# Performance work log

Hardware: AMD Instinct MI355X
Metric: run time of the kernel (lower is better)

The kernel has to match this reference:

```python
import jax, jax.numpy as jnp
import numpy as np

N1 = 100000  # layer-1 target nodes
N2 = 10000   # layer-2 target (batch) nodes
HIDDEN = 16  # hardcoded in SAGENet.__init__


def _sage_layer(x_src, src, dst, n_tgt, W, b):
    # gather neighbor messages, mean-aggregate per target, then linear
    msgs = x_src[src]                                   # [E, d]
    summed = jax.ops.segment_sum(msgs, dst, num_segments=n_tgt)  # [n_tgt, d]
    cnt = jax.ops.segment_sum(jnp.ones((src.shape[0], 1), x_src.dtype), dst,
                              num_segments=n_tgt)       # [n_tgt, 1]
    mean = summed / jnp.maximum(cnt, 1.0)
    return mean @ W + b


def setup_inputs() -> dict:
    key = jax.random.key(0)
    ks = jax.random.split(key, 9)
    in_ch, out_ch = 128, 64
    N0, E1, E2 = 500000, 2000000, 400000
    x = jax.random.normal(ks[0], (N0, in_ch), dtype=jnp.float32)
    src1 = jax.random.randint(ks[1], (E1,), 0, N0)
    dst1 = jax.random.randint(ks[2], (E1,), 0, N1)
    src2 = jax.random.randint(ks[3], (E2,), 0, N1)
    dst2 = jax.random.randint(ks[4], (E2,), 0, N2)
    # Glorot-ish init for the two SAGE linear layers
    W1 = jax.random.normal(ks[5], (in_ch, HIDDEN), dtype=jnp.float32) / np.sqrt(in_ch)
    b1 = jnp.zeros((HIDDEN,), dtype=jnp.float32)
    W2 = jax.random.normal(ks[6], (HIDDEN, out_ch), dtype=jnp.float32) / np.sqrt(HIDDEN)
    b2 = jnp.zeros((out_ch,), dtype=jnp.float32)
    return {"x": x, "W1": W1, "b1": b1, "W2": W2, "b2": b2,
            "src1": src1, "dst1": dst1, "src2": src2, "dst2": dst2}


def reference(x, W1, b1, W2, b2, src1, dst1, src2, dst2):
    # layer 1: bipartite SAGE conv (no root term since x_r is None) + relu
    h1 = jax.nn.relu(_sage_layer(x, src1, dst1, N1, W1, b1))      # [N1, 16]
    # dropout is a no-op in eval mode
    # layer 2
    h2 = _sage_layer(h1, src2, dst2, N2, W2, b2)                  # [N2, 64]
    return jax.nn.log_softmax(h2, axis=1)
```

## Files before the change

### kernel.cpp

```cpp
#include <hip/hip_runtime.h>
#include <hip/hip_bf16.h>

#define IN_CH 128
#define HID   16
#define N1_T  100000
#define N2_T  10000
#define OUT_CH 64

constexpr int PROJ_ROWS = 64;
constexpr int XS_STRIDE = 132;

__global__ __launch_bounds__(256) void proj_kernel(
    const float* __restrict__ x, const float* __restrict__ W1,
    float* __restrict__ xp, int n0) {
  __shared__ float xs[PROJ_ROWS * XS_STRIDE];

  const int tid = threadIdx.x;
  const int rowBase = blockIdx.x * PROJ_ROWS;

  const float4* x4 = reinterpret_cast<const float4*>(x + (size_t)rowBase * IN_CH);
  #pragma unroll
  for (int i = 0; i < 8; ++i) {
    int f = tid + i * 256;
    int r = f >> 5;
    int c4 = f & 31;
    if (rowBase + r < n0) {
      *reinterpret_cast<float4*>(&xs[r * XS_STRIDE + c4 * 4]) = x4[f];
    }
  }
  __syncthreads();

  const int lane = tid & 63;
  const int c0 = __builtin_amdgcn_readfirstlane((tid >> 6) << 2);

  const float* xrow = &xs[lane * XS_STRIDE];
  float a0 = 0.f, a1 = 0.f, a2 = 0.f, a3 = 0.f;
  #pragma unroll
  for (int k = 0; k < IN_CH; k += 4) {
    float4 xv = *reinterpret_cast<const float4*>(xrow + k);
    float4 w0 = *reinterpret_cast<const float4*>(W1 + (k + 0) * HID + c0);
    float4 w1 = *reinterpret_cast<const float4*>(W1 + (k + 1) * HID + c0);
    float4 w2 = *reinterpret_cast<const float4*>(W1 + (k + 2) * HID + c0);
    float4 w3 = *reinterpret_cast<const float4*>(W1 + (k + 3) * HID + c0);
    a0 += xv.x * w0.x + xv.y * w1.x + xv.z * w2.x + xv.w * w3.x;
    a1 += xv.x * w0.y + xv.y * w1.y + xv.z * w2.y + xv.w * w3.y;
    a2 += xv.x * w0.z + xv.y * w1.z + xv.z * w2.z + xv.w * w3.z;
    a3 += xv.x * w0.w + xv.y * w1.w + xv.z * w2.w + xv.w * w3.w;
  }

  const int orow = rowBase + lane;
  if (orow < n0) {
    *reinterpret_cast<float4*>(&xp[(size_t)orow * HID + c0]) =
        make_float4(a0, a1, a2, a3);
  }
}

__global__ __launch_bounds__(256) void build_list(
    const int* __restrict__ dst, int E, int* head, int* __restrict__ nxt) {
  const int stride = gridDim.x * blockDim.x;
  for (int t = blockIdx.x * blockDim.x + threadIdx.x; t < E; t += stride) {
    const int d = dst[t];
    const int old = atomicExch(&head[d], t);
    nxt[t] = old;
  }
}

__global__ __launch_bounds__(256) void agg_layer(
    const float* __restrict__ feat, const int* __restrict__ srcArr,
    const int* __restrict__ head, const int* __restrict__ nxt,
    const float* __restrict__ bias, float* __restrict__ outFeat,
    int nrows, int doReluBias) {
  const int gid = blockIdx.x * blockDim.x + threadIdx.x;
  const int row = gid >> 2;
  const int q = gid & 3;
  if (row >= nrows) return;

  int e = head[row];
  float4 acc = make_float4(0.f, 0.f, 0.f, 0.f);
  int cnt = 0;
  while (e >= 0) {
    const int s = srcArr[e];
    const float4 v =
        *reinterpret_cast<const float4*>(&feat[(size_t)s * HID + q * 4]);
    acc.x += v.x; acc.y += v.y; acc.z += v.z; acc.w += v.w;
    ++cnt;
    e = nxt[e];
  }
  const float inv = 1.0f / (float)(cnt > 0 ? cnt : 1);
  float4 r;
  r.x = acc.x * inv; r.y = acc.y * inv; r.z = acc.z * inv; r.w = acc.w * inv;
  if (doReluBias) {
    const float4 b = reinterpret_cast<const float4*>(bias)[q];
    r.x = fmaxf(r.x + b.x, 0.f);
    r.y = fmaxf(r.y + b.y, 0.f);
    r.z = fmaxf(r.z + b.z, 0.f);
    r.w = fmaxf(r.w + b.w, 0.f);
  }
  *reinterpret_cast<float4*>(&outFeat[(size_t)row * HID + q * 4]) = r;
}

__global__ __launch_bounds__(256) void out_kernel(
    const float* __restrict__ mean2, const float* __restrict__ W2,
    const float* __restrict__ b2, float* __restrict__ out, int n2) {
  const int row = blockIdx.x * 4 + (threadIdx.x >> 6);
  if (row >= n2) return;
  const int c = threadIdx.x & 63;

  float acc = b2[c];
  #pragma unroll
  for (int k = 0; k < HID; ++k) {
    acc += mean2[(size_t)row * HID + k] * W2[k * OUT_CH + c];
  }
  float mx = acc;
  #pragma unroll
  for (int off = 32; off > 0; off >>= 1) mx = fmaxf(mx, __shfl_xor(mx, off));
  float ex = expf(acc - mx);
  float sum = ex;
  #pragma unroll
  for (int off = 32; off > 0; off >>= 1) sum += __shfl_xor(sum, off);
  out[(size_t)row * OUT_CH + c] = acc - mx - logf(sum);
}

extern "C" void kernel_launch(void* const* d_in, const int* in_sizes, int n_in,
                              void* d_out, int out_size, void* d_ws, size_t ws_size,
                              hipStream_t stream) {
  const float* x   = (const float*)d_in[0];
  const float* W1  = (const float*)d_in[1];
  const float* b1  = (const float*)d_in[2];
  const float* W2  = (const float*)d_in[3];
  const float* b2  = (const float*)d_in[4];
  const int* src1  = (const int*)d_in[5];
  const int* dst1  = (const int*)d_in[6];
  const int* src2  = (const int*)d_in[7];
  const int* dst2  = (const int*)d_in[8];

  const int n0 = in_sizes[0] / IN_CH;
  const int E1 = in_sizes[5];
  const int E2 = in_sizes[7];

  float* ws    = (float*)d_ws;
  float* xp    = ws;
  float* h1    = xp + (size_t)n0 * HID;
  float* mean2 = h1 + (size_t)N1_T * HID;
  int*   head  = (int*)(mean2 + (size_t)N2_T * HID);
  int*   nxt1  = head + (N1_T + N2_T);
  int*   nxt2  = nxt1 + E1;

  float* out = (float*)d_out;

  hipMemsetAsync(head, 0xFF, (size_t)(N1_T + N2_T) * sizeof(int), stream);

  build_list<<<1024, 256, 0, stream>>>(dst1, E1, head, nxt1);
  build_list<<<256, 256, 0, stream>>>(dst2, E2, head + N1_T, nxt2);

  const int proj_blocks = (n0 + PROJ_ROWS - 1) / PROJ_ROWS;
  proj_kernel<<<proj_blocks, 256, 0, stream>>>(x, W1, xp, n0);

  agg_layer<<<(N1_T * 4 + 255) / 256, 256, 0, stream>>>(
      xp, src1, head, nxt1, b1, h1, N1_T, 1);

  agg_layer<<<(N2_T * 4 + 255) / 256, 256, 0, stream>>>(
      h1, src2, head + N1_T, nxt2, nullptr, mean2, N2_T, 0);

  out_kernel<<<(N2_T + 3) / 4, 256, 0, stream>>>(mean2, W2, b2, out, N2_T);
}
```

Baseline: 609.0 us.

## Restructure projection: stage transposed W1 in LDS, read x directly per thread

The projection kernel no longer stages x tiles in shared memory. It loads a transposed copy of W1 into LDS, and each thread reads four x rows straight from global memory to compute a 4x4 output tile. Each block now covers 256 rows instead of 64. The aim is to drop the x staging and barrier cost and to reuse weights from LDS across four rows. The risk is that lanes read x rows 512 bytes apart, so global loads may coalesce worse than the contiguous float4 tile load did.

```diff
diff --git a/kernel.cpp b/kernel.cpp
--- a/kernel.cpp
+++ b/kernel.cpp
@@ -7,52 +7,81 @@
 #define N2_T  10000
 #define OUT_CH 64
 
-constexpr int PROJ_ROWS = 64;
-constexpr int XS_STRIDE = 132;
+constexpr int WT_STRIDE = 132;
 
 __global__ __launch_bounds__(256) void proj_kernel(
     const float* __restrict__ x, const float* __restrict__ W1,
     float* __restrict__ xp, int n0) {
-  __shared__ float xs[PROJ_ROWS * XS_STRIDE];
+  __shared__ float wt[HID * WT_STRIDE];
 
   const int tid = threadIdx.x;
-  const int rowBase = blockIdx.x * PROJ_ROWS;
 
-  const float4* x4 = reinterpret_cast<const float4*>(x + (size_t)rowBase * IN_CH);
-  #pragma unroll
-  for (int i = 0; i < 8; ++i) {
-    int f = tid + i * 256;
-    int r = f >> 5;
-    int c4 = f & 31;
-    if (rowBase + r < n0) {
-      *reinterpret_cast<float4*>(&xs[r * XS_STRIDE + c4 * 4]) = x4[f];
-    }
+  if (tid < IN_CH) {
+    const float4* wrow = reinterpret_cast<const float4*>(W1 + tid * HID);
+    float4 w0 = wrow[0], w1 = wrow[1], w2 = wrow[2], w3 = wrow[3];
+    wt[ 0 * WT_STRIDE + tid] = w0.x; wt[ 1 * WT_STRIDE + tid] = w0.y;
+    wt[ 2 * WT_STRIDE + tid] = w0.z; wt[ 3 * WT_STRIDE + tid] = w0.w;
+    wt[ 4 * WT_STRIDE + tid] = w1.x; wt[ 5 * WT_STRIDE + tid] = w1.y;
+    wt[ 6 * WT_STRIDE + tid] = w1.z; wt[ 7 * WT_STRIDE + tid] = w1.w;
+    wt[ 8 * WT_STRIDE + tid] = w2.x; wt[ 9 * WT_STRIDE + tid] = w2.y;
+    wt[10 * WT_STRIDE + tid] = w2.z; wt[11 * WT_STRIDE + tid] = w2.w;
+    wt[12 * WT_STRIDE + tid] = w3.x; wt[13 * WT_STRIDE + tid] = w3.y;
+    wt[14 * WT_STRIDE + tid] = w3.z; wt[15 * WT_STRIDE + tid] = w3.w;
   }
   __syncthreads();
 
-  const int lane = tid & 63;
-  const int c0 = __builtin_amdgcn_readfirstlane((tid >> 6) << 2);
+  const int q = tid & 3;
+  const int g = tid >> 2;
+  const int r0 = blockIdx.x * 256 + g * 4;
+  if (r0 >= n0) return;
 
-  const float* xrow = &xs[lane * XS_STRIDE];
-  float a0 = 0.f, a1 = 0.f, a2 = 0.f, a3 = 0.f;
-  #pragma unroll
-  for (int k = 0; k < IN_CH; k += 4) {
-    float4 xv = *reinterpret_cast<const float4*>(xrow + k);
-    float4 w0 = *reinterpret_cast<const float4*>(W1 + (k + 0) * HID + c0);
-    float4 w1 = *reinterpret_cast<const float4*>(W1 + (k + 1) * HID + c0);
-    float4 w2 = *reinterpret_cast<const float4*>(W1 + (k + 2) * HID + c0);
-    float4 w3 = *reinterpret_cast<const float4*>(W1 + (k + 3) * HID + c0);
-    a0 += xv.x * w0.x + xv.y * w1.x + xv.z * w2.x + xv.w * w3.x;
-    a1 += xv.x * w0.y + xv.y * w1.y + xv.z * w2.y + xv.w * w3.y;
-    a2 += xv.x * w0.z + xv.y * w1.z + xv.z * w2.z + xv.w * w3.z;
-    a3 += xv.x * w0.w + xv.y * w1.w + xv.z * w2.w + xv.w * w3.w;
+  const float* wq = &wt[(q * 4) * WT_STRIDE];
+  const float* xr0 = x + (size_t)r0 * IN_CH;
+  const float* xr1 = x + (size_t)min(r0 + 1, n0 - 1) * IN_CH;
+  const float* xr2 = x + (size_t)min(r0 + 2, n0 - 1) * IN_CH;
+  const float* xr3 = x + (size_t)min(r0 + 3, n0 - 1) * IN_CH;
+
+  float4 acc0 = make_float4(0.f, 0.f, 0.f, 0.f);
+  float4 acc1 = acc0, acc2 = acc0, acc3 = acc0;
+
+  #pragma unroll 8
+  for (int kb = 0; kb < IN_CH; kb += 4) {
+    const float4 wa = *reinterpret_cast<const float4*>(wq + 0 * WT_STRIDE + kb);
+    const float4 wb = *reinterpret_cast<const float4*>(wq + 1 * WT_STRIDE + kb);
+    const float4 wc = *reinterpret_cast<const float4*>(wq + 2 * WT_STRIDE + kb);
+    const float4 wd = *reinterpret_cast<const float4*>(wq + 3 * WT_STRIDE + kb);
+    const float4 x0 = *reinterpret_cast<const float4*>(xr0 + kb);
+    const float4 x1 = *reinterpret_cast<const float4*>(xr1 + kb);
+    const float4 x2 = *reinterpret_cast<const float4*>(xr2 + kb);
+    const float4 x3 = *reinterpret_cast<const float4*>(xr3 + kb);
+
+    acc0.x += x0.x*wa.x + x0.y*wa.y + x0.z*wa.z + x0.w*wa.w;
+    acc0.y += x0.x*wb.x + x0.y*wb.y + x0.z*wb.z + x0.w*wb.w;
+    acc0.z += x0.x*wc.x + x0.y*wc.y + x0.z*wc.z + x0.w*wc.w;
+    acc0.w += x0.x*wd.x + x0.y*wd.y + x0.z*wd.z + x0.w*wd.w;
+
+    acc1.x += x1.x*wa.x + x1.y*wa.y + x1.z*wa.z + x1.w*wa.w;
+    acc1.y += x1.x*wb.x + x1.y*wb.y + x1.z*wb.z + x1.w*wb.w;
+    acc1.z += x1.x*wc.x + x1.y*wc.y + x1.z*wc.z + x1.w*wc.w;
+    acc1.w += x1.x*wd.x + x1.y*wd.y + x1.z*wd.z + x1.w*wd.w;
+
+    acc2.x += x2.x*wa.x + x2.y*wa.y + x2.z*wa.z + x2.w*wa.w;
+    acc2.y += x2.x*wb.x + x2.y*wb.y + x2.z*wb.z + x2.w*wb.w;
+    acc2.z += x2.x*wc.x + x2.y*wc.y + x2.z*wc.z + x2.w*wc.w;
+    acc2.w += x2.x*wd.x + x2.y*wd.y + x2.z*wd.z + x2.w*wd.w;
+
+    acc3.x += x3.x*wa.x + x3.y*wa.y + x3.z*wa.z + x3.w*wa.w;
+    acc3.y += x3.x*wb.x + x3.y*wb.y + x3.z*wb.z + x3.w*wb.w;
+    acc3.z += x3.x*wc.x + x3.y*wc.y + x3.z*wc.z + x3.w*wc.w;
+    acc3.w += x3.x*wd.x + x3.y*wd.y + x3.z*wd.z + x3.w*wd.w;
   }
 
-  const int orow = rowBase + lane;
-  if (orow < n0) {
-    *reinterpret_cast<float4*>(&xp[(size_t)orow * HID + c0]) =
-        make_float4(a0, a1, a2, a3);
-  }
+  float4* xpo = reinterpret_cast<float4*>(xp + (size_t)r0 * HID + q * 4);
+  const int stride4 = HID / 4;
+  xpo[0] = acc0;
+  if (r0 + 1 < n0) xpo[1 * stride4] = acc1;
+  if (r0 + 2 < n0) xpo[2 * stride4] = acc2;
+  if (r0 + 3 < n0) xpo[3 * stride4] = acc3;
 }
 
 __global__ __launch_bounds__(256) void build_list(
@@ -153,8 +182,7 @@
   build_list<<<1024, 256, 0, stream>>>(dst1, E1, head, nxt1);
   build_list<<<256, 256, 0, stream>>>(dst2, E2, head + N1_T, nxt2);
 
-  const int proj_blocks = (n0 + PROJ_ROWS - 1) / PROJ_ROWS;
-  proj_kernel<<<proj_blocks, 256, 0, stream>>>(x, W1, xp, n0);
+  proj_kernel<<<(n0 + 255) / 256, 256, 0, stream>>>(x, W1, xp, n0);
 
   agg_layer<<<(N1_T * 4 + 255) / 256, 256, 0, stream>>>(
       xp, src1, head, nxt1, b1, h1, N1_T, 1);
```

Result: no change. 610.5 us (+0.2%).
